# Kernel optimization log

Hardware: AMD Instinct MI355X
Metric: run time of the kernel (lower is better)

Reference implementation:

```python
import jax, jax.numpy as jnp
import numpy as np

B, N, D, H = 4, 1024, 1024, 16
DH = D // H  # 64
FF = 4 * D   # 4096


def _layernorm(x, w, b, eps=1e-5):
    mu = jnp.mean(x, axis=-1, keepdims=True)
    var = jnp.var(x, axis=-1, keepdims=True)
    return (x - mu) * jax.lax.rsqrt(var + eps) * w + b


def setup_inputs() -> dict:
    key = jax.random.key(0)
    ks = jax.random.split(key, 8)
    s = 0.02
    return {
        "x": jax.random.normal(ks[0], (B, N, D), jnp.float32),
        "ln1_w": jnp.ones((D,), jnp.float32),
        "ln1_b": jnp.zeros((D,), jnp.float32),
        "qkv_w": jax.random.normal(ks[1], (3 * D, D), jnp.float32) * s,
        "qkv_b": jnp.zeros((3 * D,), jnp.float32),
        "proj_l_w": jax.random.normal(ks[2], (H, H), jnp.float32) * s,
        "proj_l_b": jnp.zeros((H,), jnp.float32),
        "proj_w_w": jax.random.normal(ks[3], (H, H), jnp.float32) * s,
        "proj_w_b": jnp.zeros((H,), jnp.float32),
        "out_w": jax.random.normal(ks[4], (D, D), jnp.float32) * s,
        "out_b": jnp.zeros((D,), jnp.float32),
        "gamma1": jnp.ones((D,), jnp.float32),
        "ln2_w": jnp.ones((D,), jnp.float32),
        "ln2_b": jnp.zeros((D,), jnp.float32),
        "fc1_w": jax.random.normal(ks[5], (FF, D), jnp.float32) * s,
        "fc1_b": jnp.zeros((FF,), jnp.float32),
        "fc2_w": jax.random.normal(ks[6], (D, FF), jnp.float32) * s,
        "fc2_b": jnp.zeros((D,), jnp.float32),
        "gamma2": jnp.ones((D,), jnp.float32),
    }


def reference(x, ln1_w, ln1_b, qkv_w, qkv_b, proj_l_w, proj_l_b, proj_w_w,
              proj_w_b, out_w, out_b, gamma1, ln2_w, ln2_b, fc1_w, fc1_b,
              fc2_w, fc2_b, gamma2):
    # ---- LayerScale(TalkingHeadAttention) branch ----
    h = _layernorm(x, ln1_w, ln1_b)
    qkv = h @ qkv_w.T + qkv_b                      # [B,N,3D]
    q, k, v = jnp.split(qkv, 3, axis=-1)
    # [B,N,D] -> [B,H,N,DH]
    reshape = lambda t: t.reshape(B, N, H, DH).transpose(0, 2, 1, 3)
    q, k, v = reshape(q), reshape(k), reshape(v)
    attn = jnp.einsum("bhid,bhjd->bhij", q, k) * (DH ** -0.5)
    # talking-heads mixing before softmax (Linear over head dim)
    attn = jnp.einsum("bhij,gh->bgij", attn, proj_l_w) + proj_l_b[None, :, None, None]
    attn = jax.nn.softmax(attn, axis=-1)
    # talking-heads mixing after softmax
    attn = jnp.einsum("bhij,gh->bgij", attn, proj_w_w) + proj_w_b[None, :, None, None]
    o = jnp.einsum("bhij,bhjd->bhid", attn, v)     # [B,H,N,DH]
    o = o.transpose(0, 2, 1, 3).reshape(B, N, D)
    o = o @ out_w.T + out_b
    x = x + gamma1 * o
    # ---- LayerScale(MLP) branch ----
    h = _layernorm(x, ln2_w, ln2_b)
    h = jax.nn.gelu(h @ fc1_w.T + fc1_b)
    h = h @ fc2_w.T + fc2_b
    return x + gamma2 * h
```

## Files before the change

kernel.cpp:

```cpp
#include <hip/hip_runtime.h>


typedef _Float16 f16x8 __attribute__((ext_vector_type(8)));
typedef _Float16 f16x4 __attribute__((ext_vector_type(4)));
typedef _Float16 f16x2 __attribute__((ext_vector_type(2)));
typedef float f32x4 __attribute__((ext_vector_type(4)));

#define B_ 4
#define N_ 1024
#define D_ 1024
#define H_ 16
#define DH_ 64
#define FF_ 4096
#define M_ (B_ * N_)

__device__ __forceinline__ float gelu_act(float x) {
  float z = 0.7978845608028654f * (x + 0.044715f * x * x * x);
  return x / (1.0f + __expf(-2.0f * z));
}

__device__ __forceinline__ void ld_lds16(const _Float16* g, _Float16* l) {
  __builtin_amdgcn_global_load_lds((const __attribute__((address_space(1))) void*)g,
                                   (__attribute__((address_space(3))) void*)l, 16, 0, 0);
}

__device__ __forceinline__ int swz8(int i) {
  return (((i >> 2) << 1) ^ (i & 3)) & 7;
}
__device__ __forceinline__ int lds_off(int p, int i, int j) {
  int ch = ((j >> 3) ^ swz8(i) ^ ((p >> 2) << 1)) & 7;
  return p * 1032 + i * 64 + (ch << 3) + (j & 7);
}

__global__ __launch_bounds__(256) void cast_all(
    const float* __restrict__ a0, _Float16* __restrict__ o0,
    const float* __restrict__ a1, _Float16* __restrict__ o1,
    const float* __restrict__ a2, _Float16* __restrict__ o2,
    const float* __restrict__ a3, _Float16* __restrict__ o3,
    const float* __restrict__ W1, const float* __restrict__ W2,
    _Float16* __restrict__ w1f, _Float16* __restrict__ w2f,
    float* __restrict__ bsum) {
  int b = blockIdx.x, t = threadIdx.x;
  const float* in;
  _Float16* out;
  int base;
  if (b < 3072) { in = a0; out = o0; base = b; }
  else if (b < 4096) { in = a1; out = o1; base = b - 3072; }
  else if (b < 8192) { in = a2; out = o2; base = b - 4096; }
  else if (b < 12288) { in = a3; out = o3; base = b - 8192; }
  else {
    w1f[t] = (_Float16)W1[t];
    w2f[t] = (_Float16)W2[t];
    float4 z = {0.f, 0.f, 0.f, 0.f};
    #pragma unroll
    for (int r = 0; r < 4; r++) *(float4*)(bsum + t * 16 + r * 4) = z;
    return;
  }
  int i = (base * 256 + t) * 4;
  float4 v = *(const float4*)(in + i);
  f16x4 o;
  o[0] = (_Float16)v.x; o[1] = (_Float16)v.y; o[2] = (_Float16)v.z; o[3] = (_Float16)v.w;
  *(f16x4*)(out + i) = o;
}

__global__ __launch_bounds__(256) void ln_f16(const float* __restrict__ x,
                                              const float* __restrict__ w,
                                              const float* __restrict__ b,
                                              _Float16* __restrict__ out) {
  int row = blockIdx.x;
  int tid = threadIdx.x;
  const float* xr = x + (size_t)row * D_;
  float4 v = *(const float4*)(xr + tid * 4);
  float s = v.x + v.y + v.z + v.w;
  float sq = v.x * v.x + v.y * v.y + v.z * v.z + v.w * v.w;
  #pragma unroll
  for (int off = 32; off > 0; off >>= 1) {
    s += __shfl_down(s, off);
    sq += __shfl_down(sq, off);
  }
  __shared__ float red[8];
  int wave = tid >> 6, lane = tid & 63;
  if (lane == 0) { red[wave] = s; red[4 + wave] = sq; }
  __syncthreads();
  float ts = red[0] + red[1] + red[2] + red[3];
  float tq = red[4] + red[5] + red[6] + red[7];
  float mean = ts * (1.0f / (float)D_);
  float var = tq * (1.0f / (float)D_) - mean * mean;
  float rs = rsqrtf(var + 1e-5f);
  float4 wv = *(const float4*)(w + tid * 4);
  float4 bv = *(const float4*)(b + tid * 4);
  f16x4 o;
  o[0] = (_Float16)((v.x - mean) * rs * wv.x + bv.x);
  o[1] = (_Float16)((v.y - mean) * rs * wv.y + bv.y);
  o[2] = (_Float16)((v.z - mean) * rs * wv.z + bv.z);
  o[3] = (_Float16)((v.w - mean) * rs * wv.w + bv.w);
  *(f16x4*)(out + (size_t)row * D_ + tid * 4) = o;
}

template <int EPI, int BN, int OCC, int SWAPXY>
__global__ __launch_bounds__(256, OCC) void gemm_nt(
    const _Float16* __restrict__ A, const _Float16* __restrict__ W,
    const float* __restrict__ bias, int M, int N, int K,
    _Float16* __restrict__ outB, float* __restrict__ outF,
    const float* __restrict__ res, const float* __restrict__ gamma) {
  __shared__ _Float16 As[128 * 64];
  __shared__ _Float16 Bs[BN * 64];
  int tid = threadIdx.x;
  int wave = tid >> 6, lane = tid & 63;
  int quad = lane >> 4, l16 = lane & 15;
  int wm = wave >> 1, wn = wave & 1;
  int m0 = (SWAPXY ? blockIdx.x : blockIdx.y) * 128;
  int n0 = (SWAPXY ? blockIdx.y : blockIdx.x) * BN;
  int lrow = lane >> 3, lcol = (lane & 7) * 8;
  const int NI = (BN == 128) ? 4 : 2;
  const int WN = (BN == 128) ? 64 : 32;

  f32x4 zero = {0.f, 0.f, 0.f, 0.f};
  f32x4 acc[4][NI];
  #pragma unroll
  for (int i = 0; i < 4; i++)
    #pragma unroll
    for (int j = 0; j < NI; j++) acc[i][j] = zero;

  for (int k0 = 0; k0 < K; k0 += 64) {
    __syncthreads();
    #pragma unroll
    for (int c = 0; c < 4; c++) {
      int rb = c * 32 + wave * 8;
      ld_lds16(A + (size_t)(m0 + rb + lrow) * K + k0 + lcol, As + rb * 64);
      if (BN == 128 || c < 2)
        ld_lds16(W + (size_t)(n0 + rb + lrow) * K + k0 + lcol, Bs + rb * 64);
    }
    __syncthreads();
    #pragma unroll
    for (int ks = 0; ks < 2; ks++) {
      int kk = ks * 32 + quad * 8;
      f16x8 a[4], bfr[NI];
      #pragma unroll
      for (int i = 0; i < 4; i++) a[i] = *(const f16x8*)(As + (wm * 64 + i * 16 + l16) * 64 + kk);
      #pragma unroll
      for (int i = 0; i < NI; i++) bfr[i] = *(const f16x8*)(Bs + (wn * WN + i * 16 + l16) * 64 + kk);
      #pragma unroll
      for (int mi = 0; mi < 4; mi++)
        #pragma unroll
        for (int ni = 0; ni < NI; ni++)
          acc[mi][ni] = __builtin_amdgcn_mfma_f32_16x16x32_f16(a[mi], bfr[ni], acc[mi][ni], 0, 0, 0);
    }
  }

  #pragma unroll
  for (int mi = 0; mi < 4; mi++) {
    int grow_base = m0 + wm * 64 + mi * 16 + quad * 4;
    #pragma unroll
    for (int ni = 0; ni < NI; ni++) {
      int gcol = n0 + wn * WN + ni * 16 + l16;
      float bb = bias[gcol];
      float gm = (EPI == 1) ? gamma[gcol] : 0.f;
      #pragma unroll
      for (int r = 0; r < 4; r++) {
        size_t oi = (size_t)(grow_base + r) * N + gcol;
        float c = acc[mi][ni][r] + bb;
        if (EPI == 0) {
          outB[oi] = (_Float16)c;
        } else if (EPI == 1) {
          outF[oi] = res[oi] + gm * c;
        } else {
          outB[oi] = (_Float16)gelu_act(c);
        }
      }
    }
  }
}

#define GPH_OPEN()                                      \
  __builtin_amdgcn_sched_barrier(0);                    \
  __builtin_amdgcn_s_barrier();                         \
  asm volatile("s_waitcnt lgkmcnt(0)" ::: "memory");    \
  __builtin_amdgcn_sched_barrier(0);                    \
  __builtin_amdgcn_s_setprio(1)

#define GPH_CLOSE()                                     \
  __builtin_amdgcn_s_setprio(0);                        \
  __builtin_amdgcn_sched_barrier(0);                    \
  __builtin_amdgcn_s_barrier()

#define GPH_CLOSE_VM(n)                                 \
  __builtin_amdgcn_s_setprio(0);                        \
  __builtin_amdgcn_sched_barrier(0);                    \
  asm volatile("s_waitcnt vmcnt(" #n ")" ::: "memory"); \
  __builtin_amdgcn_s_barrier()

#define GMFMA(MB, NB)                                                         \
  _Pragma("unroll") for (int ks = 0; ks < 2; ks++)                            \
  _Pragma("unroll") for (int mi = 0; mi < 4; mi++)                            \
  _Pragma("unroll") for (int ni = 0; ni < 2; ni++)                            \
    acc[MB + mi][NB + ni] = __builtin_amdgcn_mfma_f32_16x16x32_f16(           \
        ar[mi][ks], br[NB + ni][ks], acc[MB + mi][NB + ni], 0, 0, 0)

#define LDA(buf, MB)                                            \
  _Pragma("unroll") for (int ks = 0; ks < 2; ks++)              \
  _Pragma("unroll") for (int mi = 0; mi < 4; mi++)              \
    ar[mi][ks] = rdf(&lds[buf][0][wm][0], MB + mi, ks)

#define LDB(buf, NB)                                            \
  _Pragma("unroll") for (int ks = 0; ks < 2; ks++)              \
  _Pragma("unroll") for (int ni = 0; ni < 2; ni++)              \
    br[NB + ni][ks] = rdf(&lds[buf][1][wn >> 1][0], fbB + NB + ni, ks)

template <int EPI>
__global__ __launch_bounds__(512, 2) void gemm_nt8(
    const _Float16* __restrict__ A, const _Float16* __restrict__ W,
    const float* __restrict__ bias, int M, int N, int K,
    _Float16* __restrict__ outB) {
  __shared__ _Float16 lds[2][2][2][8192];
  const int tid = threadIdx.x;
  const int wv = tid >> 6, lane = tid & 63;
  const int quad = lane >> 4, l16 = lane & 15;
  const int wm = wv >> 2, wn = wv & 3;
  const int fbB = (wn & 1) * 4;
  const int wg = ((int)blockIdx.x & 7) * ((int)gridDim.x >> 3) + ((int)blockIdx.x >> 3);
  const int m0 = (wg & 15) << 8;
  const int n0 = (wg >> 4) << 8;
  const int gc = ((lane & 7) ^ (lane >> 3)) << 3;
  const int srow = wv * 8 + (lane >> 3);

  auto stageA = [&](int kt, int h) {
    const _Float16* g = A + (size_t)(m0 + h * 128 + srow) * K + kt * 64 + gc;
    _Float16* l = &lds[kt & 1][0][h][wv * 512];
    ld_lds16(g, l);
    ld_lds16(g + (size_t)64 * K, l + 4096);
  };
  auto stageB = [&](int kt, int h) {
    const _Float16* g = W + (size_t)(n0 + h * 128 + srow) * K + kt * 64 + gc;
    _Float16* l = &lds[kt & 1][1][h][wv * 512];
    ld_lds16(g, l);
    ld_lds16(g + (size_t)64 * K, l + 4096);
  };
  auto rdf = [&](const _Float16* base, int fi, int ks) -> f16x8 {
    int row = fi * 16 + l16;
    int pc = ((ks << 2) + quad) ^ (l16 & 7);
    return *(const f16x8*)(base + row * 64 + (pc << 3));
  };

  f32x4 acc[8][4];
  const f32x4 zero = {0.f, 0.f, 0.f, 0.f};
  #pragma unroll
  for (int i = 0; i < 8; i++)
    #pragma unroll
    for (int j = 0; j < 4; j++) acc[i][j] = zero;
  f16x8 ar[4][2], br[4][2];

  stageA(0, 0); stageA(0, 1); stageB(0, 0); stageB(0, 1);
  stageB(1, 0); stageB(1, 1);
  asm volatile("s_waitcnt vmcnt(4)" ::: "memory");
  __builtin_amdgcn_s_barrier();

  const int NT = K >> 6;
  const int ITERS = NT >> 1;
  for (int it = 0; it < ITERS - 1; ++it) {
    const int t0 = it * 2;
    LDA(0, 0); LDB(0, 0); stageA(t0 + 1, 0);
    GPH_OPEN(); GMFMA(0, 0); GPH_CLOSE();
    LDB(0, 2); stageA(t0 + 1, 1);
    GPH_OPEN(); GMFMA(0, 2); GPH_CLOSE();
    LDA(0, 4); stageB(t0 + 2, 0);
    GPH_OPEN(); GMFMA(4, 0); GPH_CLOSE();
    stageB(t0 + 2, 1);
    GPH_OPEN(); GMFMA(4, 2); GPH_CLOSE_VM(4);
    LDA(1, 0); LDB(1, 0); stageA(t0 + 2, 0);
    GPH_OPEN(); GMFMA(0, 0); GPH_CLOSE();
    LDB(1, 2); stageA(t0 + 2, 1);
    GPH_OPEN(); GMFMA(0, 2); GPH_CLOSE();
    LDA(1, 4); stageB(t0 + 3, 0);
    GPH_OPEN(); GMFMA(4, 0); GPH_CLOSE();
    stageB(t0 + 3, 1);
    GPH_OPEN(); GMFMA(4, 2); GPH_CLOSE_VM(4);
  }
  {
    LDA(0, 0); LDB(0, 0); stageA(NT - 1, 0);
    GPH_OPEN(); GMFMA(0, 0); GPH_CLOSE();
    LDB(0, 2); stageA(NT - 1, 1);
    GPH_OPEN(); GMFMA(0, 2); GPH_CLOSE();
    LDA(0, 4);
    GPH_OPEN(); GMFMA(4, 0); GPH_CLOSE();
    GPH_OPEN(); GMFMA(4, 2); GPH_CLOSE_VM(0);
    LDA(1, 0); LDB(1, 0);
    GPH_OPEN(); GMFMA(0, 0); GPH_CLOSE();
    LDB(1, 2);
    GPH_OPEN(); GMFMA(0, 2); GPH_CLOSE();
    LDA(1, 4);
    GPH_OPEN(); GMFMA(4, 0); GPH_CLOSE();
    GPH_OPEN(); GMFMA(4, 2); GPH_CLOSE();
  }

  #pragma unroll
  for (int mi = 0; mi < 8; mi++) {
    int grow = m0 + wm * 128 + mi * 16 + quad * 4;
    #pragma unroll
    for (int ni = 0; ni < 4; ni++) {
      int gcol = n0 + wn * 64 + ni * 16 + l16;
      float bb = bias[gcol];
      #pragma unroll
      for (int r = 0; r < 4; r++) {
        size_t oi = (size_t)(grow + r) * N + gcol;
        float c = acc[mi][ni][r] + bb;
        outB[oi] = (_Float16)(EPI == 2 ? gelu_act(c) : c);
      }
    }
  }
}

__global__ __launch_bounds__(256) void transpose_v(const _Float16* __restrict__ qkv,
                                                   _Float16* __restrict__ vt,
                                                   const float* __restrict__ b2,
                                                   float* __restrict__ bsum) {
  int jt = blockIdx.x;
  int h = blockIdx.y;
  int b = blockIdx.z;
  __shared__ _Float16 tl[64][68];
  int tid = threadIdx.x;
  int j0 = jt * 64;
  #pragma unroll
  for (int k = 0; k < 16; k++) {
    int idx = k * 256 + tid;
    int jr = idx >> 6, dc = idx & 63;
    tl[jr][dc] = qkv[(size_t)(b * N_ + j0 + jr) * (3 * D_) + 2 * D_ + h * 64 + dc];
  }
  __syncthreads();
  #pragma unroll
  for (int k = 0; k < 16; k++) {
    int idx = k * 256 + tid;
    int dr = idx >> 6, jc = idx & 63;
    vt[(size_t)((b * H_ + h) * DH_ + dr) * N_ + j0 + jc] = tl[jc][dr];
  }
  int d = tid & 63, jq = tid >> 6;
  float s = 0.f;
  #pragma unroll
  for (int r = 0; r < 16; r++) s += (float)tl[jq * 16 + r][d];
  atomicAdd(&bsum[b * D_ + h * 64 + d], b2[h] * s);
}

__global__ __launch_bounds__(1024, 4) void attn_th(
    const _Float16* __restrict__ qkv, const _Float16* __restrict__ vt,
    const _Float16* __restrict__ w1f, const _Float16* __restrict__ w2f,
    const float* __restrict__ b1f, const float* __restrict__ bsum,
    _Float16* __restrict__ ob) {
  __shared__ __align__(16) _Float16 SP[2 * 16512];
  __shared__ float lsum[272];
  _Float16* Sp = SP;
  _Float16* Pp = SP + 16512;

  const int tid = threadIdx.x;
  const int wave = tid >> 6;
  const int lane = tid & 63;
  const int quad = lane >> 4, l16 = lane & 15;
  const int i0 = blockIdx.y * 16;
  const int b = blockIdx.x;
  const size_t bN = (size_t)b * N_;
  const f32x4 zero = {0.f, 0.f, 0.f, 0.f};

  f16x8 qf[2];
  #pragma unroll
  for (int ks = 0; ks < 2; ks++) {
    f16x8 q = *(const f16x8*)(qkv + (bN + i0 + l16) * 3072 + wave * 64 + ks * 32 + quad * 8);
    #pragma unroll
    for (int e = 0; e < 8; e++) q[e] = q[e] * (_Float16)0.125f;
    qf[ks] = q;
  }
  f16x4 w1a = *(const f16x4*)(w1f + l16 * 16 + quad * 4);
  float b1v = b1f[l16];
  f32x4 b1i = {b1v, b1v, b1v, b1v};

  const _Float16* vbase = vt + (size_t)((b * H_ + wave) * DH_ + l16) * N_ + quad * 8;

  f32x4 uacc[4];
  #pragma unroll
  for (int nt = 0; nt < 4; nt++) uacc[nt] = zero;
  float lacc = 0.f;

  f16x8 kcur[4][2];
  auto loadK = [&](int j0) {
    #pragma unroll
    for (int jb = 0; jb < 4; jb++) {
      const _Float16* kb = qkv + (bN + j0 + jb * 16 + l16) * 3072 + 1024 + wave * 64 + quad * 8;
      kcur[jb][0] = *(const f16x8*)kb;
      kcur[jb][1] = *(const f16x8*)(kb + 32);
    }
  };
  loadK(0);

  f16x8 vreg[4];

  for (int t = 0; t < 16; t++) {
    int j0 = t * 64;
    f32x4 sres[4];
    #pragma unroll
    for (int jb = 0; jb < 4; jb++) {
      f32x4 s = __builtin_amdgcn_mfma_f32_16x16x32_f16(kcur[jb][0], qf[0], zero, 0, 0, 0);
      sres[jb] = __builtin_amdgcn_mfma_f32_16x16x32_f16(kcur[jb][1], qf[1], s, 0, 0, 0);
    }
    #pragma unroll
    for (int jb = 0; jb < 4; jb++) {
      f16x4 sv;
      #pragma unroll
      for (int r = 0; r < 4; r++) sv[r] = (_Float16)sres[jb][r];
      *(f16x4*)(Sp + lds_off(wave, l16, jb * 16 + quad * 4)) = sv;
    }
    if (t < 15) loadK(j0 + 64);
    #pragma unroll
    for (int nt = 0; nt < 4; nt++)
      vreg[nt] = *(const f16x8*)(vbase + (size_t)(nt * 16) * N_ + j0);
    __syncthreads();
    #pragma unroll
    for (int cg = 0; cg < 4; cg++) {
      f16x4 sf;
      #pragma unroll
      for (int t4 = 0; t4 < 4; t4++)
        sf[t4] = Sp[lds_off(quad * 4 + t4, wave, cg * 16 + l16)];
      f32x4 a = __builtin_amdgcn_mfma_f32_16x16x16f16(sf, w1a, b1i, 0, 0, 0);
      f16x4 pv;
      #pragma unroll
      for (int r = 0; r < 4; r++) {
        float e = __expf(a[r]);
        lacc += e;
        pv[r] = (_Float16)e;
      }
      *(f16x4*)(Pp + lds_off(l16, wave, cg * 16 + quad * 4)) = pv;
    }
    __syncthreads();
    f16x8 pf0 = *(const f16x8*)(Pp + lds_off(wave, l16, quad * 8));
    f16x8 pf1 = *(const f16x8*)(Pp + lds_off(wave, l16, 32 + quad * 8));
    #pragma unroll
    for (int nt = 0; nt < 4; nt++)
      uacc[nt] = __builtin_amdgcn_mfma_f32_16x16x32_f16(vreg[nt], pf0, uacc[nt], 0, 0, 0);
    #pragma unroll
    for (int nt = 0; nt < 4; nt++) {
      f16x8 vf = *(const f16x8*)(vbase + (size_t)(nt * 16) * N_ + j0 + 32);
      uacc[nt] = __builtin_amdgcn_mfma_f32_16x16x32_f16(vf, pf1, uacc[nt], 0, 0, 0);
    }
  }

  lacc += __shfl_xor(lacc, 16);
  lacc += __shfl_xor(lacc, 32);
  __syncthreads();
  if (quad == 0) lsum[l16 * 17 + wave] = lacc;
  __syncthreads();
  float invl = 1.0f / lsum[wave * 17 + l16];

  _Float16* Uf = Sp;
  #pragma unroll
  for (int nt = 0; nt < 4; nt++) {
    f16x4 u;
    #pragma unroll
    for (int r = 0; r < 4; r++) u[r] = (_Float16)(uacc[nt][r] * invl);
    *(f16x4*)(Uf + wave * 1092 + l16 * 68 + nt * 16 + quad * 4) = u;
  }
  __syncthreads();

  f16x4 w2a = *(const f16x4*)(w2f + l16 * 16 + quad * 4);
  #pragma unroll
  for (int cg = 0; cg < 4; cg++) {
    f16x4 af;
    #pragma unroll
    for (int t4 = 0; t4 < 4; t4++)
      af[t4] = Uf[(quad * 4 + t4) * 1092 + wave * 68 + cg * 16 + l16];
    f32x4 o = __builtin_amdgcn_mfma_f32_16x16x16f16(af, w2a, zero, 0, 0, 0);
    f32x4 bs = *(const f32x4*)(bsum + b * D_ + l16 * 64 + cg * 16 + quad * 4);
    f16x4 ov;
    #pragma unroll
    for (int r = 0; r < 4; r++) ov[r] = (_Float16)(o[r] + bs[r]);
    *(f16x4*)(ob + (bN + i0 + wave) * D_ + l16 * 64 + cg * 16 + quad * 4) = ov;
  }
}

extern "C" void kernel_launch(void* const* d_in, const int* in_sizes, int n_in,
                              void* d_out, int out_size, void* d_ws, size_t ws_size,
                              hipStream_t stream) {
  const float* x      = (const float*)d_in[0];
  const float* ln1_w  = (const float*)d_in[1];
  const float* ln1_b  = (const float*)d_in[2];
  const float* qkv_w  = (const float*)d_in[3];
  const float* qkv_b  = (const float*)d_in[4];
  const float* plw    = (const float*)d_in[5];
  const float* plb    = (const float*)d_in[6];
  const float* pww    = (const float*)d_in[7];
  const float* pwb    = (const float*)d_in[8];
  const float* out_w  = (const float*)d_in[9];
  const float* out_b  = (const float*)d_in[10];
  const float* gamma1 = (const float*)d_in[11];
  const float* ln2_w  = (const float*)d_in[12];
  const float* ln2_b  = (const float*)d_in[13];
  const float* fc1_w  = (const float*)d_in[14];
  const float* fc1_b  = (const float*)d_in[15];
  const float* fc2_w  = (const float*)d_in[16];
  const float* fc2_b  = (const float*)d_in[17];
  const float* gamma2 = (const float*)d_in[18];
  float* out = (float*)d_out;

  char* ws = (char*)d_ws;
  _Float16* wq   = (_Float16*)(ws + 0);
  _Float16* wo   = (_Float16*)(ws + 6291456);
  _Float16* wf1  = (_Float16*)(ws + 8388608);
  _Float16* wf2  = (_Float16*)(ws + 16777216);
  float*    x1   = (float*)   (ws + 25165824);
  _Float16* ob   = (_Float16*)(ws + 41943040);
  _Float16* hb   = (_Float16*)(ws + 50331648);
  _Float16* qkvb = (_Float16*)(ws + 58720256);
  _Float16* vtb  = (_Float16*)(ws + 83886080);
  _Float16* fb   = (_Float16*)(ws + 58720256);
  _Float16* w1f  = (_Float16*)(ws + 25165824);
  _Float16* w2f  = (_Float16*)(ws + 25165824 + 512);
  float*    bsum = (float*)   (ws + 25165824 + 1024);
  if (ws_size < 92274688) return;

  cast_all<<<12289, 256, 0, stream>>>(qkv_w, wq, out_w, wo, fc1_w, wf1, fc2_w, wf2,
                                      plw, pww, w1f, w2f, bsum);

  ln_f16<<<4096, 256, 0, stream>>>(x, ln1_w, ln1_b, hb);
  gemm_nt8<0><<<192, 512, 0, stream>>>(hb, wq, qkv_b, M_, 3 * D_, D_, qkvb);
  transpose_v<<<dim3(16, 16, 4), 256, 0, stream>>>(qkvb, vtb, pwb, bsum);
  attn_th<<<dim3(4, 64), 1024, 0, stream>>>(qkvb, vtb, w1f, w2f, plb, bsum, ob);
  gemm_nt<1, 64, 4, 1><<<dim3(32, 16), 256, 0, stream>>>(ob, wo, out_b, M_, D_, D_, nullptr, x1, x, gamma1);

  ln_f16<<<4096, 256, 0, stream>>>(x1, ln2_w, ln2_b, hb);
  gemm_nt8<2><<<256, 512, 0, stream>>>(hb, wf1, fc1_b, M_, FF_, D_, fb);
  gemm_nt<1, 128, 3, 1><<<dim3(32, 8), 256, 0, stream>>>(fb, wf2, fc2_b, M_, D_, FF_, nullptr, out, x1, gamma2);
}
```

Before: 449.0 us.

## Split-K the fc2 GEMM onto the 256x256 MFMA kernel with a combine pass

The fc2 GEMM (K=4096) now runs on the large-tile gemm_nt8 kernel with a 4-way split-K, so 256 workgroups each handle 16 K-tiles and write fp16 partials into reused workspace regions. A new combine kernel sums the four partials and applies bias, the gamma2 scale and the residual add. The aim is to fill the GPU with the faster tiled kernel instead of the smaller gemm_nt launch. In exchange it adds partial-sum traffic and an extra launch, and rounds the partials to fp16, which costs some precision. NT is now hardcoded to 16, which is correct because the QKV and fc1 GEMMs both have K=1024.

```diff
diff --git a/kernel.cpp b/kernel.cpp
--- a/kernel.cpp
+++ b/kernel.cpp
@@ -211,7 +211,7 @@
 __global__ __launch_bounds__(512, 2) void gemm_nt8(
     const _Float16* __restrict__ A, const _Float16* __restrict__ W,
     const float* __restrict__ bias, int M, int N, int K,
-    _Float16* __restrict__ outB) {
+    _Float16* __restrict__ outB, _Float16* __restrict__ outB2) {
   __shared__ _Float16 lds[2][2][2][8192];
   const int tid = threadIdx.x;
   const int wv = tid >> 6, lane = tid & 63;
@@ -219,20 +219,29 @@
   const int wm = wv >> 2, wn = wv & 3;
   const int fbB = (wn & 1) * 4;
   const int wg = ((int)blockIdx.x & 7) * ((int)gridDim.x >> 3) + ((int)blockIdx.x >> 3);
-  const int m0 = (wg & 15) << 8;
-  const int n0 = (wg >> 4) << 8;
+  int split = 0, kt0 = 0, m0, n0;
+  if (EPI == 3) {
+    split = wg >> 6;
+    int rem = wg & 63;
+    m0 = (rem & 15) << 8;
+    n0 = (rem >> 4) << 8;
+    kt0 = split << 4;
+  } else {
+    m0 = (wg & 15) << 8;
+    n0 = (wg >> 4) << 8;
+  }
   const int gc = ((lane & 7) ^ (lane >> 3)) << 3;
   const int srow = wv * 8 + (lane >> 3);
 
-  auto stageA = [&](int kt, int h) {
-    const _Float16* g = A + (size_t)(m0 + h * 128 + srow) * K + kt * 64 + gc;
-    _Float16* l = &lds[kt & 1][0][h][wv * 512];
+  auto stageA = [&](int lt, int h) {
+    const _Float16* g = A + (size_t)(m0 + h * 128 + srow) * K + (kt0 + lt) * 64 + gc;
+    _Float16* l = &lds[lt & 1][0][h][wv * 512];
     ld_lds16(g, l);
     ld_lds16(g + (size_t)64 * K, l + 4096);
   };
-  auto stageB = [&](int kt, int h) {
-    const _Float16* g = W + (size_t)(n0 + h * 128 + srow) * K + kt * 64 + gc;
-    _Float16* l = &lds[kt & 1][1][h][wv * 512];
+  auto stageB = [&](int lt, int h) {
+    const _Float16* g = W + (size_t)(n0 + h * 128 + srow) * K + (kt0 + lt) * 64 + gc;
+    _Float16* l = &lds[lt & 1][1][h][wv * 512];
     ld_lds16(g, l);
     ld_lds16(g + (size_t)64 * K, l + 4096);
   };
@@ -255,7 +264,7 @@
   asm volatile("s_waitcnt vmcnt(4)" ::: "memory");
   __builtin_amdgcn_s_barrier();
 
-  const int NT = K >> 6;
+  const int NT = 16;
   const int ITERS = NT >> 1;
   for (int it = 0; it < ITERS - 1; ++it) {
     const int t0 = it * 2;
@@ -293,21 +302,46 @@
     GPH_OPEN(); GMFMA(4, 2); GPH_CLOSE();
   }
 
+  _Float16* po = outB;
+  if (EPI == 3)
+    po = (split < 2 ? outB : outB2) + (size_t)(split & 1) * ((size_t)M * N);
   #pragma unroll
   for (int mi = 0; mi < 8; mi++) {
     int grow = m0 + wm * 128 + mi * 16 + quad * 4;
     #pragma unroll
     for (int ni = 0; ni < 4; ni++) {
       int gcol = n0 + wn * 64 + ni * 16 + l16;
-      float bb = bias[gcol];
+      float bb = (EPI == 3) ? 0.f : bias[gcol];
       #pragma unroll
       for (int r = 0; r < 4; r++) {
         size_t oi = (size_t)(grow + r) * N + gcol;
         float c = acc[mi][ni][r] + bb;
-        outB[oi] = (_Float16)(EPI == 2 ? gelu_act(c) : c);
+        po[oi] = (_Float16)(EPI == 2 ? gelu_act(c) : c);
       }
     }
   }
+}
+
+__global__ __launch_bounds__(256) void fc2_combine(
+    const _Float16* __restrict__ p01, const _Float16* __restrict__ p23,
+    const float* __restrict__ x1, const float* __restrict__ gamma,
+    const float* __restrict__ bias, float* __restrict__ out) {
+  const size_t idx = ((size_t)blockIdx.x * 256 + threadIdx.x) * 4;
+  const int col = (int)(idx & (D_ - 1));
+  const size_t soff = (size_t)M_ * D_;
+  f16x4 a = *(const f16x4*)(p01 + idx);
+  f16x4 b = *(const f16x4*)(p01 + soff + idx);
+  f16x4 c = *(const f16x4*)(p23 + idx);
+  f16x4 d = *(const f16x4*)(p23 + soff + idx);
+  float4 xv = *(const float4*)(x1 + idx);
+  float4 gv = *(const float4*)(gamma + col);
+  float4 bv = *(const float4*)(bias + col);
+  float4 o;
+  o.x = xv.x + gv.x * ((float)a[0] + (float)b[0] + (float)c[0] + (float)d[0] + bv.x);
+  o.y = xv.y + gv.y * ((float)a[1] + (float)b[1] + (float)c[1] + (float)d[1] + bv.y);
+  o.z = xv.z + gv.z * ((float)a[2] + (float)b[2] + (float)c[2] + (float)d[2] + bv.z);
+  o.w = xv.w + gv.w * ((float)a[3] + (float)b[3] + (float)c[3] + (float)d[3] + bv.w);
+  *(float4*)(out + idx) = o;
 }
 
 __global__ __launch_bounds__(256) void transpose_v(const _Float16* __restrict__ qkv,
@@ -511,18 +545,21 @@
   _Float16* w1f  = (_Float16*)(ws + 25165824);
   _Float16* w2f  = (_Float16*)(ws + 25165824 + 512);
   float*    bsum = (float*)   (ws + 25165824 + 1024);
+  _Float16* p01  = (_Float16*)(ws + 0);
+  _Float16* p23  = (_Float16*)(ws + 41943040);
   if (ws_size < 92274688) return;
 
   cast_all<<<12289, 256, 0, stream>>>(qkv_w, wq, out_w, wo, fc1_w, wf1, fc2_w, wf2,
                                       plw, pww, w1f, w2f, bsum);
 
   ln_f16<<<4096, 256, 0, stream>>>(x, ln1_w, ln1_b, hb);
-  gemm_nt8<0><<<192, 512, 0, stream>>>(hb, wq, qkv_b, M_, 3 * D_, D_, qkvb);
+  gemm_nt8<0><<<192, 512, 0, stream>>>(hb, wq, qkv_b, M_, 3 * D_, D_, qkvb, nullptr);
   transpose_v<<<dim3(16, 16, 4), 256, 0, stream>>>(qkvb, vtb, pwb, bsum);
   attn_th<<<dim3(4, 64), 1024, 0, stream>>>(qkvb, vtb, w1f, w2f, plb, bsum, ob);
   gemm_nt<1, 64, 4, 1><<<dim3(32, 16), 256, 0, stream>>>(ob, wo, out_b, M_, D_, D_, nullptr, x1, x, gamma1);
 
   ln_f16<<<4096, 256, 0, stream>>>(x1, ln2_w, ln2_b, hb);
-  gemm_nt8<2><<<256, 512, 0, stream>>>(hb, wf1, fc1_b, M_, FF_, D_, fb);
-  gemm_nt<1, 128, 3, 1><<<dim3(32, 8), 256, 0, stream>>>(fb, wf2, fc2_b, M_, D_, FF_, nullptr, out, x1, gamma2);
-}
+  gemm_nt8<2><<<256, 512, 0, stream>>>(hb, wf1, fc1_b, M_, FF_, D_, fb, nullptr);
+  gemm_nt8<3><<<256, 512, 0, stream>>>(fb, wf2, fc2_b, M_, D_, FF_, p01, p23);
+  fc2_combine<<<4096, 256, 0, stream>>>(p01, p23, x1, gamma2, fc2_b, out);
+}
```

New measurement: 427.0 us. -4.9%, faster.
